# Performance work log

Hardware: AMD Instinct MI355X
Metric: run time of the kernel (lower is better)

The kernel has to match this reference:

```python
import jax, jax.numpy as jnp
import numpy as np

VOCAB, D_IN, D_H = 32000, 512, 1024
B, T = 16, 256
PAD_IDX = 0


def setup_inputs() -> dict:
    key = jax.random.key(0)
    k1, k2, k3, k4, k5 = jax.random.split(key, 5)
    input_idx = jax.random.randint(k1, (B, T), 0, VOCAB, dtype=jnp.int64)
    emb = jax.random.normal(k2, (VOCAB, D_IN), dtype=jnp.float32) * 0.02
    emb = emb.at[PAD_IDX].set(0.0)  # padding_idx row is zero
    weight_x = jax.random.normal(k3, (D_H, D_IN), dtype=jnp.float32) * (1.0 / np.sqrt(D_IN))
    weight_h = jax.random.normal(k4, (D_H, D_H), dtype=jnp.float32) * (1.0 / np.sqrt(D_H))
    bias = jnp.zeros((D_H,), dtype=jnp.float32)
    lm_W = jax.random.normal(k5, (VOCAB, D_H), dtype=jnp.float32) * (1.0 / np.sqrt(D_H))
    return {"input_idx": input_idx, "emb": emb, "weight_x": weight_x,
            "weight_h": weight_h, "bias": bias, "lm_W": lm_W}


def reference(input_idx, emb, weight_x, weight_h, bias, lm_W):
    Bsz = input_idx.shape[0]
    h0 = jnp.zeros((Bsz, weight_h.shape[0]), dtype=weight_x.dtype)

    def step(h, tok):
        x = emb[tok]  # [B, D_IN]
        h_new = jnp.tanh(x @ weight_x.T + h @ weight_h.T + bias)
        mask = (tok != PAD_IDX)[:, None]  # keep old h at pad positions
        h = jnp.where(mask, h_new, h)
        return h, h

    _, h_all = jax.lax.scan(step, h0, input_idx.T)  # [T, B, H]
    h_all = jnp.swapaxes(h_all, 0, 1)               # [B, T, H]
    logits = jnp.einsum('bth,vh->btv', h_all, lm_W)  # [B, T, V]
    return logits
```

## Files before the change

kernel.cpp:

```cpp
#include <hip/hip_runtime.h>

#define PAD_IDX 0

typedef __attribute__((ext_vector_type(8))) short short8;
typedef __attribute__((ext_vector_type(4))) float f32x4;

__device__ __forceinline__ unsigned short f32_to_bf16_rne(float f) {
  unsigned int u = __builtin_bit_cast(unsigned int, f);
  u += 0x7FFFu + ((u >> 16) & 1u);
  return (unsigned short)(u >> 16);
}

__device__ __forceinline__ void load16_to_lds(const void* g, void* lds) {
  __builtin_amdgcn_global_load_lds(
      (const __attribute__((address_space(1))) unsigned int*)g,
      (__attribute__((address_space(3))) unsigned int*)lds,
      16, 0, 0);
}

__global__ void sentinel_kernel(float* out) { out[0] = 1.0e6f; }

__global__ __launch_bounds__(256) void xwcvt_kernel(const int* __restrict__ tok,
                                                    const float* __restrict__ emb,
                                                    const float* __restrict__ Wx,
                                                    const float* __restrict__ bias,
                                                    float* __restrict__ xw,
                                                    const float* __restrict__ lmW,
                                                    unsigned short* __restrict__ lmW_bf) {
  int tid = threadIdx.x;
  if (blockIdx.x >= 1024) {
    const int n8 = 32000 * 1024 / 8;
    int stride = 512 * 256;
    for (int i = (blockIdx.x - 1024) * 256 + tid; i < n8; i += stride) {
      float4 a = ((const float4*)lmW)[2 * i];
      float4 b = ((const float4*)lmW)[2 * i + 1];
      ushort4 lo, hi;
      lo.x = f32_to_bf16_rne(a.x); lo.y = f32_to_bf16_rne(a.y);
      lo.z = f32_to_bf16_rne(a.z); lo.w = f32_to_bf16_rne(a.w);
      hi.x = f32_to_bf16_rne(b.x); hi.y = f32_to_bf16_rne(b.y);
      hi.z = f32_to_bf16_rne(b.z); hi.w = f32_to_bf16_rne(b.w);
      ((ushort4*)lmW_bf)[2 * i] = lo;
      ((ushort4*)lmW_bf)[2 * i + 1] = hi;
    }
    return;
  }
  __shared__ float At[32][68];
  __shared__ float Bt[32][68];
  __shared__ int stok[64];
  int tm = blockIdx.x & 63;
  int tn = blockIdx.x >> 6;
  int r0 = tm * 64, j0 = tn * 64;
  if (tid < 64) stok[tid] = tok[r0 + tid];
  int tx = tid & 15, ty = tid >> 4;
  float acc[4][4] = {};
  for (int kt = 0; kt < 512; kt += 32) {
    __syncthreads();
    #pragma unroll
    for (int ii = 0; ii < 2; ++ii) {
      int idx = tid * 2 + ii;
      int m = idx >> 3, fv = idx & 7;
      float4 va = *(const float4*)&emb[(size_t)stok[m] * 512 + kt + fv * 4];
      float4 vb = *(const float4*)&Wx[(size_t)(j0 + m) * 512 + kt + fv * 4];
      At[fv * 4 + 0][m] = va.x; At[fv * 4 + 1][m] = va.y;
      At[fv * 4 + 2][m] = va.z; At[fv * 4 + 3][m] = va.w;
      Bt[fv * 4 + 0][m] = vb.x; Bt[fv * 4 + 1][m] = vb.y;
      Bt[fv * 4 + 2][m] = vb.z; Bt[fv * 4 + 3][m] = vb.w;
    }
    __syncthreads();
    #pragma unroll
    for (int k = 0; k < 32; ++k) {
      float4 a4 = *(const float4*)&At[k][ty * 4];
      float4 b4 = *(const float4*)&Bt[k][tx * 4];
      float av[4] = {a4.x, a4.y, a4.z, a4.w};
      float bv[4] = {b4.x, b4.y, b4.z, b4.w};
      #pragma unroll
      for (int i = 0; i < 4; ++i)
        #pragma unroll
        for (int jj = 0; jj < 4; ++jj) acc[i][jj] = fmaf(av[i], bv[jj], acc[i][jj]);
    }
  }
  #pragma unroll
  for (int i = 0; i < 4; ++i) {
    size_t row = (size_t)(r0 + ty * 4 + i) * 1024 + j0 + tx * 4;
    #pragma unroll
    for (int jj = 0; jj < 4; ++jj)
      xw[row + jj] = acc[i][jj] + bias[j0 + tx * 4 + jj];
  }
}

__global__ __launch_bounds__(1024, 4) void rec_kernel(const float* __restrict__ Wh,
                                                      const float* __restrict__ xw,
                                                      const int* __restrict__ tok,
                                                      unsigned long long* hcomb,
                                                      unsigned short* __restrict__ h_all) {
  int c = blockIdx.x & 15;
  int g = blockIdx.x >> 4;
  int tid = threadIdx.x;
  int w = tid >> 6;
  int l = tid & 63;
  int j = g * 64 + l;

  const float* wb = Wh + (size_t)j * 1024 + w * 64;
#define LDW(i) f32x4 w##i = *(const f32x4*)(wb + i * 4);
  LDW(0) LDW(1) LDW(2) LDW(3) LDW(4) LDW(5) LDW(6) LDW(7)
  LDW(8) LDW(9) LDW(10) LDW(11) LDW(12) LDW(13) LDW(14) LDW(15)
#undef LDW

  __shared__ float hs[16][64];
  __shared__ float pbuf[16][64];
  unsigned long long* hc0 = hcomb + (size_t)c * 1024;
  unsigned long long* hc1 = hcomb + 16 * 1024 + (size_t)c * 1024;
  bool writer = (w == 0);
  float prevh = 0.f;

  for (int t = 0; t < 256; ++t) {
    float xv = 0.f;
    int tkn = 1;
    if (writer) {
      xv = xw[((size_t)c * 256 + t) * 1024 + j];
      tkn = tok[c * 256 + t];
    }
    unsigned long long* src = ((t & 1) ? hc1 : hc0) + tid;
    unsigned long long v;
    int guard = 0;
    do {
      v = __hip_atomic_load(src, __ATOMIC_RELAXED, __HIP_MEMORY_SCOPE_AGENT);
      if ((unsigned int)(v >> 32) == (unsigned int)t) break;
      __builtin_amdgcn_s_sleep(1);
    } while (++guard < (1 << 20));
    hs[w][l] = __builtin_bit_cast(float, (unsigned int)v);
    __asm__ volatile("s_waitcnt lgkmcnt(0)" ::: "memory");

    const float* hp = &hs[w][0];
    f32x4 a0 = {0.f, 0.f, 0.f, 0.f}, a1 = a0, a2 = a0, a3 = a0;
#define FMAI(i, acc) { f32x4 h4 = *(const f32x4*)(hp + i * 4); acc += w##i * h4; }
    FMAI(0, a0) FMAI(1, a1) FMAI(2, a2) FMAI(3, a3)
    FMAI(4, a0) FMAI(5, a1) FMAI(6, a2) FMAI(7, a3)
    FMAI(8, a0) FMAI(9, a1) FMAI(10, a2) FMAI(11, a3)
    FMAI(12, a0) FMAI(13, a1) FMAI(14, a2) FMAI(15, a3)
#undef FMAI
    f32x4 aa = (a0 + a1) + (a2 + a3);
    pbuf[w][l] = (aa[0] + aa[1]) + (aa[2] + aa[3]);
    __asm__ volatile("s_waitcnt lgkmcnt(0)\n\ts_barrier" ::: "memory");

    if (writer) {
      float s = 0.f;
      #pragma unroll
      for (int q = 0; q < 16; ++q) s += pbuf[q][l];
      float hnew;
      if (tkn != PAD_IDX) {
        float pre = xv + s;
        float e = __builtin_amdgcn_exp2f(pre * 2.8853900817779268f);
        hnew = 1.0f - 2.0f / (e + 1.0f);
      } else {
        hnew = prevh;
      }
      prevh = hnew;
      unsigned long long pv =
          ((unsigned long long)(unsigned int)(t + 1) << 32) |
          (unsigned long long)__builtin_bit_cast(unsigned int, hnew);
      __hip_atomic_store((((t + 1) & 1) ? hc1 : hc0) + j, pv,
                         __ATOMIC_RELAXED, __HIP_MEMORY_SCOPE_AGENT);
      h_all[((size_t)c * 256 + t) * 1024 + j] = f32_to_bf16_rne(hnew);
    }
  }
}

__global__ __launch_bounds__(512) void gemm_kernel(const unsigned short* __restrict__ A,
                                                   const unsigned short* __restrict__ B,
                                                   float* __restrict__ C) {
  __shared__ unsigned short lds[2 * 32768];
  int tid = threadIdx.x;
  int lane = tid & 63, wave = tid >> 6;
  int bid = blockIdx.x;
  int wgid = (bid & 7) * 250 + (bid >> 3);
  int tm = wgid & 15, tn = wgid >> 4;
  int r0 = tm * 256, c0 = tn * 256;
  int wm = wave >> 2, wn = wave & 3;

  auto STAGE = [&](int kt, int st) {
    unsigned short* bufA = (unsigned short*)lds + st * 32768;
    unsigned short* bufB = bufA + 16384;
    #pragma unroll
    for (int i = 0; i < 4; ++i) {
      int slot = i * 512 + tid;
      int row = slot >> 3, sg = slot & 7;
      int kg = sg ^ (row & 7);
      const unsigned short* ga = A + (size_t)(r0 + row) * 1024 + kt * 64 + kg * 8;
      load16_to_lds(ga, &bufA[(i * 512 + wave * 64) * 8]);
    }
    #pragma unroll
    for (int i = 0; i < 4; ++i) {
      int slot = i * 512 + tid;
      int row = slot >> 3, sg = slot & 7;
      int kg = sg ^ (row & 7);
      const unsigned short* gb = B + (size_t)(c0 + row) * 1024 + kt * 64 + kg * 8;
      load16_to_lds(gb, &bufB[(i * 512 + wave * 64) * 8]);
    }
  };

  f32x4 zero = {0.f, 0.f, 0.f, 0.f};
  f32x4 acc[8][4];
  #pragma unroll
  for (int i = 0; i < 8; ++i)
    #pragma unroll
    for (int jx = 0; jx < 4; ++jx) acc[i][jx] = zero;

  STAGE(0, 0);
  STAGE(1, 1);
  __asm__ volatile("s_waitcnt vmcnt(8)\n\ts_barrier" ::: "memory");

  for (int kt = 0; kt < 16; ++kt) {
    int st = kt & 1;
    const unsigned short* bufA = (const unsigned short*)lds + st * 32768;
    const unsigned short* bufB = bufA + 16384;

    short8 af[8][2], bf[4][2];
    #pragma unroll
    for (int kkb = 0; kkb < 2; ++kkb) {
      int kbyte = kkb * 64 + (lane >> 4) * 16;
      #pragma unroll
      for (int i = 0; i < 8; ++i) {
        int rowa = wm * 128 + i * 16 + (lane & 15);
        af[i][kkb] = *(const short8*)((const char*)bufA + rowa * 128 + (kbyte ^ ((rowa & 7) << 4)));
      }
      #pragma unroll
      for (int i = 0; i < 4; ++i) {
        int rowb = wn * 64 + i * 16 + (lane & 15);
        bf[i][kkb] = *(const short8*)((const char*)bufB + rowb * 128 + (kbyte ^ ((rowb & 7) << 4)));
      }
    }
    __asm__ volatile("s_waitcnt lgkmcnt(0)\n\ts_barrier" ::: "memory");
    if (kt < 14) {
      STAGE(kt + 2, st);
    } else {
      unsigned short* dead = (unsigned short*)lds + st * 32768;
      #pragma unroll
      for (int i = 0; i < 8; ++i) load16_to_lds(A + (size_t)r0 * 1024, &dead[i * 8]);
    }
    __builtin_amdgcn_s_setprio(1);
    #pragma unroll
    for (int kkb = 0; kkb < 2; ++kkb)
      #pragma unroll
      for (int i = 0; i < 8; ++i)
        #pragma unroll
        for (int jx = 0; jx < 4; ++jx)
          acc[i][jx] = __builtin_amdgcn_mfma_f32_16x16x32_bf16(af[i][kkb], bf[jx][kkb], acc[i][jx], 0, 0, 0);
    __builtin_amdgcn_s_setprio(0);
    __asm__ volatile("s_waitcnt vmcnt(8)\n\ts_barrier" ::: "memory");
  }
  __asm__ volatile("s_waitcnt vmcnt(0)" ::: "memory");

  int rbase = r0 + wm * 128 + (lane >> 4) * 4;
  int cbase = c0 + wn * 64 + (lane & 15);
  #pragma unroll
  for (int i = 0; i < 8; ++i)
    #pragma unroll
    for (int jx = 0; jx < 4; ++jx)
      #pragma unroll
      for (int q = 0; q < 4; ++q)
        C[(size_t)(rbase + i * 16 + q) * 32000 + cbase + jx * 16] = acc[i][jx][q];
}

extern "C" void kernel_launch(void* const* d_in, const int* in_sizes, int n_in,
                              void* d_out, int out_size, void* d_ws, size_t ws_size,
                              hipStream_t stream) {
  const int* tok = (const int*)d_in[0];
  const float* emb = (const float*)d_in[1];
  const float* Wx = (const float*)d_in[2];
  const float* Wh = (const float*)d_in[3];
  const float* bias = (const float*)d_in[4];
  const float* lmW = (const float*)d_in[5];
  float* out = (float*)d_out;

  const size_t OFF_LMW = 0;
  const size_t OFF_XW = 65536000;
  const size_t OFF_HALL = OFF_XW + 16777216;
  const size_t OFF_HCMB = OFF_HALL + 8388608;
  const size_t NEED = OFF_HCMB + 262144;
  if (ws_size < NEED) {
    sentinel_kernel<<<1, 1, 0, stream>>>(out);
    return;
  }
  char* ws = (char*)d_ws;
  unsigned short* lmW_bf = (unsigned short*)(ws + OFF_LMW);
  float* xw = (float*)(ws + OFF_XW);
  unsigned short* h_all = (unsigned short*)(ws + OFF_HALL);
  unsigned long long* hcomb = (unsigned long long*)(ws + OFF_HCMB);

  hipMemsetAsync(ws + OFF_HCMB, 0, 262144, stream);
  xwcvt_kernel<<<1536, 256, 0, stream>>>(tok, emb, Wx, bias, xw, lmW, lmW_bf);
  rec_kernel<<<256, 1024, 0, stream>>>(Wh, xw, tok, hcomb, h_all);
  gemm_kernel<<<2000, 512, 0, stream>>>(h_all, lmW_bf, out);
}
```

Baseline: 879.1 us.

## Overlap lm_W bf16 conversion with latency-bound recurrence steps

Moves the lm_W fp32-to-bf16 conversion out of the xw precompute kernel and spreads it over the first 32 timesteps of the recurrent kernel, so it runs in the idle time while threads spin-wait on the hidden-state handoff. The xw/token loads are moved after the spin wait. The GEMM block-to-tile mapping is also changed so that consecutive blocks on each XCD share B tiles across paired M tiles. The risk is that the extra memory traffic slows the serial recurrence critical path.

```diff
diff --git a/kernel.cpp b/kernel.cpp
--- a/kernel.cpp
+++ b/kernel.cpp
@@ -20,33 +20,15 @@
 
 __global__ void sentinel_kernel(float* out) { out[0] = 1.0e6f; }
 
-__global__ __launch_bounds__(256) void xwcvt_kernel(const int* __restrict__ tok,
-                                                    const float* __restrict__ emb,
-                                                    const float* __restrict__ Wx,
-                                                    const float* __restrict__ bias,
-                                                    float* __restrict__ xw,
-                                                    const float* __restrict__ lmW,
-                                                    unsigned short* __restrict__ lmW_bf) {
-  int tid = threadIdx.x;
-  if (blockIdx.x >= 1024) {
-    const int n8 = 32000 * 1024 / 8;
-    int stride = 512 * 256;
-    for (int i = (blockIdx.x - 1024) * 256 + tid; i < n8; i += stride) {
-      float4 a = ((const float4*)lmW)[2 * i];
-      float4 b = ((const float4*)lmW)[2 * i + 1];
-      ushort4 lo, hi;
-      lo.x = f32_to_bf16_rne(a.x); lo.y = f32_to_bf16_rne(a.y);
-      lo.z = f32_to_bf16_rne(a.z); lo.w = f32_to_bf16_rne(a.w);
-      hi.x = f32_to_bf16_rne(b.x); hi.y = f32_to_bf16_rne(b.y);
-      hi.z = f32_to_bf16_rne(b.z); hi.w = f32_to_bf16_rne(b.w);
-      ((ushort4*)lmW_bf)[2 * i] = lo;
-      ((ushort4*)lmW_bf)[2 * i + 1] = hi;
-    }
-    return;
-  }
+__global__ __launch_bounds__(256) void xw_kernel(const int* __restrict__ tok,
+                                                 const float* __restrict__ emb,
+                                                 const float* __restrict__ Wx,
+                                                 const float* __restrict__ bias,
+                                                 float* __restrict__ xw) {
   __shared__ float At[32][68];
   __shared__ float Bt[32][68];
   __shared__ int stok[64];
+  int tid = threadIdx.x;
   int tm = blockIdx.x & 63;
   int tn = blockIdx.x >> 6;
   int r0 = tm * 64, j0 = tn * 64;
@@ -92,7 +74,9 @@
                                                       const float* __restrict__ xw,
                                                       const int* __restrict__ tok,
                                                       unsigned long long* hcomb,
-                                                      unsigned short* __restrict__ h_all) {
+                                                      unsigned short* __restrict__ h_all,
+                                                      const float* __restrict__ lmW,
+                                                      unsigned short* __restrict__ lmW_bf) {
   int c = blockIdx.x & 15;
   int g = blockIdx.x >> 4;
   int tid = threadIdx.x;
@@ -114,12 +98,6 @@
   float prevh = 0.f;
 
   for (int t = 0; t < 256; ++t) {
-    float xv = 0.f;
-    int tkn = 1;
-    if (writer) {
-      xv = xw[((size_t)c * 256 + t) * 1024 + j];
-      tkn = tok[c * 256 + t];
-    }
     unsigned long long* src = ((t & 1) ? hc1 : hc0) + tid;
     unsigned long long v;
     int guard = 0;
@@ -128,6 +106,21 @@
       if ((unsigned int)(v >> 32) == (unsigned int)t) break;
       __builtin_amdgcn_s_sleep(1);
     } while (++guard < (1 << 20));
+
+    float xv = 0.f;
+    int tkn = 1;
+    if (writer) {
+      xv = xw[((size_t)c * 256 + t) * 1024 + j];
+      tkn = tok[c * 256 + t];
+    }
+    float4 cva;
+    size_t fi = 0;
+    bool do_cvt = false;
+    if (t < 32) {
+      fi = (size_t)t * 262144 + ((size_t)blockIdx.x << 10) + tid;
+      if (fi < 8192000) { cva = ((const float4*)lmW)[fi]; do_cvt = true; }
+    }
+
     hs[w][l] = __builtin_bit_cast(float, (unsigned int)v);
     __asm__ volatile("s_waitcnt lgkmcnt(0)" ::: "memory");
 
@@ -141,6 +134,13 @@
 #undef FMAI
     f32x4 aa = (a0 + a1) + (a2 + a3);
     pbuf[w][l] = (aa[0] + aa[1]) + (aa[2] + aa[3]);
+
+    if (do_cvt) {
+      ushort4 o;
+      o.x = f32_to_bf16_rne(cva.x); o.y = f32_to_bf16_rne(cva.y);
+      o.z = f32_to_bf16_rne(cva.z); o.w = f32_to_bf16_rne(cva.w);
+      ((ushort4*)lmW_bf)[fi] = o;
+    }
     __asm__ volatile("s_waitcnt lgkmcnt(0)\n\ts_barrier" ::: "memory");
 
     if (writer) {
@@ -173,8 +173,10 @@
   int tid = threadIdx.x;
   int lane = tid & 63, wave = tid >> 6;
   int bid = blockIdx.x;
-  int wgid = (bid & 7) * 250 + (bid >> 3);
-  int tm = wgid & 15, tn = wgid >> 4;
+  int x = bid & 7;
+  int r = bid >> 3;
+  int tm = 2 * x + (r & 1);
+  int tn = r >> 1;
   int r0 = tm * 256, c0 = tn * 256;
   int wm = wave >> 2, wn = wave & 3;
 
@@ -289,7 +291,7 @@
   unsigned long long* hcomb = (unsigned long long*)(ws + OFF_HCMB);
 
   hipMemsetAsync(ws + OFF_HCMB, 0, 262144, stream);
-  xwcvt_kernel<<<1536, 256, 0, stream>>>(tok, emb, Wx, bias, xw, lmW, lmW_bf);
-  rec_kernel<<<256, 1024, 0, stream>>>(Wh, xw, tok, hcomb, h_all);
+  xw_kernel<<<1024, 256, 0, stream>>>(tok, emb, Wx, bias, xw);
+  rec_kernel<<<256, 1024, 0, stream>>>(Wh, xw, tok, hcomb, h_all, lmW, lmW_bf);
   gemm_kernel<<<2000, 512, 0, stream>>>(h_all, lmW_bf, out);
 }
```

Result: no change. 873.9 us (-0.6%).

## Fuse recurrence and LM-head GEMM into one kernel with progress-counter overlap

Applied to the files above, without the earlier changes.

Merges the recurrent kernel and the output GEMM into a single launch. The first 256 blocks run the recurrence and bump a per-8-timestep progress counter. The remaining blocks each compute a 128x128 GEMM tile and spin-wait until the timestep chunk they need is complete. h_all is stored time-major so that each 128-row tile maps to 8 timesteps, and the GEMM output rows are remapped back to batch-major. The aim is to hide the GEMM behind the serial recurrence, at the cost of smaller, less efficient GEMM tiles, half-idle 1024-thread GEMM blocks, and spinning blocks that may compete with the recurrence for CU resources.

```diff
diff --git a/kernel.cpp b/kernel.cpp
--- a/kernel.cpp
+++ b/kernel.cpp
@@ -88,101 +88,122 @@
   }
 }
 
-__global__ __launch_bounds__(1024, 4) void rec_kernel(const float* __restrict__ Wh,
-                                                      const float* __restrict__ xw,
-                                                      const int* __restrict__ tok,
-                                                      unsigned long long* hcomb,
-                                                      unsigned short* __restrict__ h_all) {
-  int c = blockIdx.x & 15;
-  int g = blockIdx.x >> 4;
+__global__ __launch_bounds__(1024) void recgemm_kernel(const float* __restrict__ Wh,
+                                                       const float* __restrict__ xw,
+                                                       const int* __restrict__ tok,
+                                                       unsigned long long* hcomb,
+                                                       unsigned short* h_all,
+                                                       const unsigned short* __restrict__ Bm,
+                                                       float* __restrict__ C,
+                                                       unsigned int* prog) {
+  __shared__ __align__(16) char smem[65536];
+  int bid = blockIdx.x;
   int tid = threadIdx.x;
-  int w = tid >> 6;
-  int l = tid & 63;
-  int j = g * 64 + l;
-
-  const float* wb = Wh + (size_t)j * 1024 + w * 64;
+
+  if (bid < 256) {
+    int c = bid & 15;
+    int g = bid >> 4;
+    int w = tid >> 6;
+    int l = tid & 63;
+    int j = g * 64 + l;
+
+    const float* wb = Wh + (size_t)j * 1024 + w * 64;
 #define LDW(i) f32x4 w##i = *(const f32x4*)(wb + i * 4);
-  LDW(0) LDW(1) LDW(2) LDW(3) LDW(4) LDW(5) LDW(6) LDW(7)
-  LDW(8) LDW(9) LDW(10) LDW(11) LDW(12) LDW(13) LDW(14) LDW(15)
+    LDW(0) LDW(1) LDW(2) LDW(3) LDW(4) LDW(5) LDW(6) LDW(7)
+    LDW(8) LDW(9) LDW(10) LDW(11) LDW(12) LDW(13) LDW(14) LDW(15)
 #undef LDW
 
-  __shared__ float hs[16][64];
-  __shared__ float pbuf[16][64];
-  unsigned long long* hc0 = hcomb + (size_t)c * 1024;
-  unsigned long long* hc1 = hcomb + 16 * 1024 + (size_t)c * 1024;
-  bool writer = (w == 0);
-  float prevh = 0.f;
-
-  for (int t = 0; t < 256; ++t) {
-    float xv = 0.f;
-    int tkn = 1;
-    if (writer) {
-      xv = xw[((size_t)c * 256 + t) * 1024 + j];
-      tkn = tok[c * 256 + t];
-    }
-    unsigned long long* src = ((t & 1) ? hc1 : hc0) + tid;
-    unsigned long long v;
-    int guard = 0;
-    do {
-      v = __hip_atomic_load(src, __ATOMIC_RELAXED, __HIP_MEMORY_SCOPE_AGENT);
-      if ((unsigned int)(v >> 32) == (unsigned int)t) break;
+    float* hs = (float*)smem;
+    float* pbuf = hs + 16 * 64;
+    unsigned long long* hc0 = hcomb + (size_t)c * 1024;
+    unsigned long long* hc1 = hcomb + 16 * 1024 + (size_t)c * 1024;
+    bool writer = (w == 0);
+    float prevh = 0.f;
+
+    for (int t = 0; t < 256; ++t) {
+      float xv = 0.f;
+      int tkn = 1;
+      if (writer) {
+        xv = xw[((size_t)c * 256 + t) * 1024 + j];
+        tkn = tok[c * 256 + t];
+      }
+      unsigned long long* src = ((t & 1) ? hc1 : hc0) + tid;
+      unsigned long long v;
+      int guard = 0;
+      do {
+        v = __hip_atomic_load(src, __ATOMIC_RELAXED, __HIP_MEMORY_SCOPE_AGENT);
+        if ((unsigned int)(v >> 32) == (unsigned int)t) break;
+        __builtin_amdgcn_s_sleep(1);
+      } while (++guard < (1 << 20));
+      hs[w * 64 + l] = __builtin_bit_cast(float, (unsigned int)v);
+      __asm__ volatile("s_waitcnt lgkmcnt(0)" ::: "memory");
+
+      const float* hp = hs + w * 64;
+      f32x4 a0 = {0.f, 0.f, 0.f, 0.f}, a1 = a0, a2 = a0, a3 = a0;
+#define FMAI(i, acc) { f32x4 h4 = *(const f32x4*)(hp + i * 4); acc += w##i * h4; }
+      FMAI(0, a0) FMAI(1, a1) FMAI(2, a2) FMAI(3, a3)
+      FMAI(4, a0) FMAI(5, a1) FMAI(6, a2) FMAI(7, a3)
+      FMAI(8, a0) FMAI(9, a1) FMAI(10, a2) FMAI(11, a3)
+      FMAI(12, a0) FMAI(13, a1) FMAI(14, a2) FMAI(15, a3)
+#undef FMAI
+      f32x4 aa = (a0 + a1) + (a2 + a3);
+      pbuf[w * 64 + l] = (aa[0] + aa[1]) + (aa[2] + aa[3]);
+      __asm__ volatile("s_waitcnt lgkmcnt(0)\n\ts_barrier" ::: "memory");
+
+      if (writer) {
+        float s = 0.f;
+        #pragma unroll
+        for (int q = 0; q < 16; ++q) s += pbuf[q * 64 + l];
+        float hnew;
+        if (tkn != PAD_IDX) {
+          float pre = xv + s;
+          float e = __builtin_amdgcn_exp2f(pre * 2.8853900817779268f);
+          hnew = 1.0f - 2.0f / (e + 1.0f);
+        } else {
+          hnew = prevh;
+        }
+        prevh = hnew;
+        unsigned long long pv =
+            ((unsigned long long)(unsigned int)(t + 1) << 32) |
+            (unsigned long long)__builtin_bit_cast(unsigned int, hnew);
+        __hip_atomic_store((((t + 1) & 1) ? hc1 : hc0) + j, pv,
+                           __ATOMIC_RELAXED, __HIP_MEMORY_SCOPE_AGENT);
+        h_all[((size_t)t * 16 + c) * 1024 + j] = f32_to_bf16_rne(hnew);
+        if ((t & 7) == 7) {
+          __threadfence();
+          if (tid == 0)
+            __hip_atomic_fetch_add(prog + (t >> 3), 1u,
+                                   __ATOMIC_RELAXED, __HIP_MEMORY_SCOPE_AGENT);
+        }
+      }
+    }
+    return;
+  }
+
+  if (tid >= 512) return;
+  int gb = bid - 256;
+  int mtile = gb / 250, ntile = gb - mtile * 250;
+  int r0 = mtile * 128, c0 = ntile * 128;
+  int lane = tid & 63, wave = tid >> 6;
+  int wm = wave >> 2, wn = wave & 3;
+
+  {
+    long guard = 0;
+    while (__hip_atomic_load(prog + mtile, __ATOMIC_RELAXED, __HIP_MEMORY_SCOPE_AGENT) < 256u) {
       __builtin_amdgcn_s_sleep(1);
-    } while (++guard < (1 << 20));
-    hs[w][l] = __builtin_bit_cast(float, (unsigned int)v);
-    __asm__ volatile("s_waitcnt lgkmcnt(0)" ::: "memory");
-
-    const float* hp = &hs[w][0];
-    f32x4 a0 = {0.f, 0.f, 0.f, 0.f}, a1 = a0, a2 = a0, a3 = a0;
-#define FMAI(i, acc) { f32x4 h4 = *(const f32x4*)(hp + i * 4); acc += w##i * h4; }
-    FMAI(0, a0) FMAI(1, a1) FMAI(2, a2) FMAI(3, a3)
-    FMAI(4, a0) FMAI(5, a1) FMAI(6, a2) FMAI(7, a3)
-    FMAI(8, a0) FMAI(9, a1) FMAI(10, a2) FMAI(11, a3)
-    FMAI(12, a0) FMAI(13, a1) FMAI(14, a2) FMAI(15, a3)
-#undef FMAI
-    f32x4 aa = (a0 + a1) + (a2 + a3);
-    pbuf[w][l] = (aa[0] + aa[1]) + (aa[2] + aa[3]);
-    __asm__ volatile("s_waitcnt lgkmcnt(0)\n\ts_barrier" ::: "memory");
-
-    if (writer) {
-      float s = 0.f;
-      #pragma unroll
-      for (int q = 0; q < 16; ++q) s += pbuf[q][l];
-      float hnew;
-      if (tkn != PAD_IDX) {
-        float pre = xv + s;
-        float e = __builtin_amdgcn_exp2f(pre * 2.8853900817779268f);
-        hnew = 1.0f - 2.0f / (e + 1.0f);
-      } else {
-        hnew = prevh;
-      }
-      prevh = hnew;
-      unsigned long long pv =
-          ((unsigned long long)(unsigned int)(t + 1) << 32) |
-          (unsigned long long)__builtin_bit_cast(unsigned int, hnew);
-      __hip_atomic_store((((t + 1) & 1) ? hc1 : hc0) + j, pv,
-                         __ATOMIC_RELAXED, __HIP_MEMORY_SCOPE_AGENT);
-      h_all[((size_t)c * 256 + t) * 1024 + j] = f32_to_bf16_rne(hnew);
-    }
-  }
-}
-
-__global__ __launch_bounds__(512) void gemm_kernel(const unsigned short* __restrict__ A,
-                                                   const unsigned short* __restrict__ B,
-                                                   float* __restrict__ C) {
-  __shared__ unsigned short lds[2 * 32768];
-  int tid = threadIdx.x;
-  int lane = tid & 63, wave = tid >> 6;
-  int bid = blockIdx.x;
-  int wgid = (bid & 7) * 250 + (bid >> 3);
-  int tm = wgid & 15, tn = wgid >> 4;
-  int r0 = tm * 256, c0 = tn * 256;
-  int wm = wave >> 2, wn = wave & 3;
+      if (++guard > (1L << 24)) break;
+    }
+  }
+  __threadfence();
+
+  unsigned short* ldsb = (unsigned short*)smem;
+  const unsigned short* A = h_all;
 
   auto STAGE = [&](int kt, int st) {
-    unsigned short* bufA = (unsigned short*)lds + st * 32768;
-    unsigned short* bufB = bufA + 16384;
-    #pragma unroll
-    for (int i = 0; i < 4; ++i) {
+    unsigned short* bufA = ldsb + st * 16384;
+    unsigned short* bufB = bufA + 8192;
+    #pragma unroll
+    for (int i = 0; i < 2; ++i) {
       int slot = i * 512 + tid;
       int row = slot >> 3, sg = slot & 7;
       int kg = sg ^ (row & 7);
@@ -190,43 +211,43 @@
       load16_to_lds(ga, &bufA[(i * 512 + wave * 64) * 8]);
     }
     #pragma unroll
-    for (int i = 0; i < 4; ++i) {
+    for (int i = 0; i < 2; ++i) {
       int slot = i * 512 + tid;
       int row = slot >> 3, sg = slot & 7;
       int kg = sg ^ (row & 7);
-      const unsigned short* gb = B + (size_t)(c0 + row) * 1024 + kt * 64 + kg * 8;
-      load16_to_lds(gb, &bufB[(i * 512 + wave * 64) * 8]);
+      const unsigned short* gb2 = Bm + (size_t)(c0 + row) * 1024 + kt * 64 + kg * 8;
+      load16_to_lds(gb2, &bufB[(i * 512 + wave * 64) * 8]);
     }
   };
 
   f32x4 zero = {0.f, 0.f, 0.f, 0.f};
-  f32x4 acc[8][4];
+  f32x4 acc[4][2];
   #pragma unroll
-  for (int i = 0; i < 8; ++i)
-    #pragma unroll
-    for (int jx = 0; jx < 4; ++jx) acc[i][jx] = zero;
+  for (int i = 0; i < 4; ++i)
+    #pragma unroll
+    for (int jx = 0; jx < 2; ++jx) acc[i][jx] = zero;
 
   STAGE(0, 0);
   STAGE(1, 1);
-  __asm__ volatile("s_waitcnt vmcnt(8)\n\ts_barrier" ::: "memory");
+  __asm__ volatile("s_waitcnt vmcnt(4)\n\ts_barrier" ::: "memory");
 
   for (int kt = 0; kt < 16; ++kt) {
     int st = kt & 1;
-    const unsigned short* bufA = (const unsigned short*)lds + st * 32768;
-    const unsigned short* bufB = bufA + 16384;
-
-    short8 af[8][2], bf[4][2];
+    const unsigned short* bufA = ldsb + st * 16384;
+    const unsigned short* bufB = bufA + 8192;
+
+    short8 af[4][2], bf[2][2];
     #pragma unroll
     for (int kkb = 0; kkb < 2; ++kkb) {
       int kbyte = kkb * 64 + (lane >> 4) * 16;
       #pragma unroll
-      for (int i = 0; i < 8; ++i) {
-        int rowa = wm * 128 + i * 16 + (lane & 15);
+      for (int i = 0; i < 4; ++i) {
+        int rowa = wm * 64 + i * 16 + (lane & 15);
         af[i][kkb] = *(const short8*)((const char*)bufA + rowa * 128 + (kbyte ^ ((rowa & 7) << 4)));
       }
       #pragma unroll
-      for (int i = 0; i < 4; ++i) {
-        int rowb = wn * 64 + i * 16 + (lane & 15);
+      for (int i = 0; i < 2; ++i) {
+        int rowb = wn * 32 + i * 16 + (lane & 15);
         bf[i][kkb] = *(const short8*)((const char*)bufB + rowb * 128 + (kbyte ^ ((rowb & 7) << 4)));
       }
     }
@@ -234,32 +255,35 @@
     if (kt < 14) {
       STAGE(kt + 2, st);
     } else {
-      unsigned short* dead = (unsigned short*)lds + st * 32768;
-      #pragma unroll
-      for (int i = 0; i < 8; ++i) load16_to_lds(A + (size_t)r0 * 1024, &dead[i * 8]);
+      unsigned short* dead = ldsb + st * 16384;
+      #pragma unroll
+      for (int i = 0; i < 4; ++i) load16_to_lds(A + (size_t)r0 * 1024, &dead[i * 8]);
     }
     __builtin_amdgcn_s_setprio(1);
     #pragma unroll
     for (int kkb = 0; kkb < 2; ++kkb)
       #pragma unroll
-      for (int i = 0; i < 8; ++i)
+      for (int i = 0; i < 4; ++i)
         #pragma unroll
-        for (int jx = 0; jx < 4; ++jx)
+        for (int jx = 0; jx < 2; ++jx)
           acc[i][jx] = __builtin_amdgcn_mfma_f32_16x16x32_bf16(af[i][kkb], bf[jx][kkb], acc[i][jx], 0, 0, 0);
     __builtin_amdgcn_s_setprio(0);
-    __asm__ volatile("s_waitcnt vmcnt(8)\n\ts_barrier" ::: "memory");
+    __asm__ volatile("s_waitcnt vmcnt(4)\n\ts_barrier" ::: "memory");
   }
   __asm__ volatile("s_waitcnt vmcnt(0)" ::: "memory");
 
-  int rbase = r0 + wm * 128 + (lane >> 4) * 4;
-  int cbase = c0 + wn * 64 + (lane & 15);
+  int rbase = r0 + wm * 64 + (lane >> 4) * 4;
+  int cbase = c0 + wn * 32 + (lane & 15);
   #pragma unroll
-  for (int i = 0; i < 8; ++i)
-    #pragma unroll
-    for (int jx = 0; jx < 4; ++jx)
-      #pragma unroll
-      for (int q = 0; q < 4; ++q)
-        C[(size_t)(rbase + i * 16 + q) * 32000 + cbase + jx * 16] = acc[i][jx][q];
+  for (int i = 0; i < 4; ++i)
+    #pragma unroll
+    for (int jx = 0; jx < 2; ++jx)
+      #pragma unroll
+      for (int q = 0; q < 4; ++q) {
+        int R = rbase + i * 16 + q;
+        int Crow = (R & 15) * 256 + (R >> 4);
+        C[(size_t)Crow * 32000 + cbase + jx * 16] = acc[i][jx][q];
+      }
 }
 
 extern "C" void kernel_launch(void* const* d_in, const int* in_sizes, int n_in,
@@ -277,7 +301,8 @@
   const size_t OFF_XW = 65536000;
   const size_t OFF_HALL = OFF_XW + 16777216;
   const size_t OFF_HCMB = OFF_HALL + 8388608;
-  const size_t NEED = OFF_HCMB + 262144;
+  const size_t OFF_PROG = OFF_HCMB + 262144;
+  const size_t NEED = OFF_PROG + 128;
   if (ws_size < NEED) {
     sentinel_kernel<<<1, 1, 0, stream>>>(out);
     return;
@@ -287,9 +312,10 @@
   float* xw = (float*)(ws + OFF_XW);
   unsigned short* h_all = (unsigned short*)(ws + OFF_HALL);
   unsigned long long* hcomb = (unsigned long long*)(ws + OFF_HCMB);
-
-  hipMemsetAsync(ws + OFF_HCMB, 0, 262144, stream);
+  unsigned int* prog = (unsigned int*)(ws + OFF_PROG);
+
+  hipMemsetAsync(ws + OFF_HCMB, 0, 262144 + 128, stream);
   xwcvt_kernel<<<1536, 256, 0, stream>>>(tok, emb, Wx, bias, xw, lmW, lmW_bf);
-  rec_kernel<<<256, 1024, 0, stream>>>(Wh, xw, tok, hcomb, h_all);
-  gemm_kernel<<<2000, 512, 0, stream>>>(h_all, lmW_bf, out);
-}
+  recgemm_kernel<<<256 + 8000, 1024, 0, stream>>>(Wh, xw, tok, hcomb, h_all,
+                                                  lmW_bf, out, prog);
+}
```

Result: slower. 3.247 ms (+269.4%).
